# Kernel tuning notes

Hardware: AMD Instinct MI355X
Metric: run time of the kernel (lower is better)

## Reference

```python
import jax, jax.numpy as jnp
import numpy as np

B, LK, D = 32, 2048, 32          # batch, key seq len, input feature dim
LQ = 128                          # number of reference query time points
ET, H = 128, 8                    # embed_time, num_heads
ETK = ET // H
NH = 128                          # nhidden


def setup_inputs() -> dict:
    key = jax.random.key(0)
    ks = jax.random.split(key, 24)
    g = lambda k, shape: jax.random.normal(k, shape, dtype=jnp.float32) * 0.05
    inp = {
        "x": jax.random.normal(ks[0], (B, LK, D), dtype=jnp.float32),
        "time_steps": jax.random.uniform(ks[1], (B, LK), dtype=jnp.float32),
        "query_times": jnp.linspace(0.0, 1.0, LQ, dtype=jnp.float32),
        # learned time embedding: linear(1->1) and periodic(1->ET-1)
        "Wlin": g(ks[2], (1, 1)), "blin": g(ks[3], (1,)),
        "Wper": g(ks[4], (ET - 1, 1)), "bper": g(ks[5], (ET - 1,)),
        # attention projections
        "Wq": g(ks[6], (ET, ET)), "bq": g(ks[7], (ET,)),
        "Wk": g(ks[8], (ET, ET)), "bk": g(ks[9], (ET,)),
        "Wo": g(ks[10], (NH, D * H)), "bo": g(ks[11], (NH,)),
        # GRU (single layer, input NH -> hidden NH), gate order r,z,n
        "W_ih": g(ks[12], (3 * NH, NH)), "b_ih": g(ks[13], (3 * NH,)),
        "W_hh": g(ks[14], (3 * NH, NH)), "b_hh": g(ks[15], (3 * NH,)),
        # classifier MLP NH->300->300->2
        "W1": g(ks[16], (300, NH)), "b1": g(ks[17], (300,)),
        "W2": g(ks[18], (300, 300)), "b2": g(ks[19], (300,)),
        "W3": g(ks[20], (2, 300)), "b3": g(ks[21], (2,)),
    }
    return inp


def _time_embed(tt, Wlin, blin, Wper, bper):
    # tt: (..., L) -> (..., L, ET)
    t = tt[..., None]
    out1 = t @ Wlin.T + blin                  # (..., L, 1)
    out2 = jnp.sin(t @ Wper.T + bper)         # (..., L, ET-1)
    return jnp.concatenate([out1, out2], axis=-1)


def reference(x, time_steps, query_times, Wlin, blin, Wper, bper,
              Wq, bq, Wk, bk, Wo, bo,
              W_ih, b_ih, W_hh, b_hh,
              W1, b1, W2, b2, W3, b3):
    # time embeddings
    k_emb = _time_embed(time_steps, Wlin, blin, Wper, bper)       # (B, LK, ET)
    q_emb = _time_embed(query_times[None, :], Wlin, blin, Wper, bper)  # (1, LQ, ET)

    # multi-head projections
    q = (q_emb @ Wq.T + bq).reshape(1, LQ, H, ETK).transpose(0, 2, 1, 3)   # (1,H,LQ,ETK)
    k = (k_emb @ Wk.T + bk).reshape(B, LK, H, ETK).transpose(0, 2, 1, 3)   # (B,H,LK,ETK)

    # scores broadcast over batch; softmax over keys. Repeating scores over the
    # value feature dim then summing (original code) is mathematically identical
    # to softmax(scores) @ value.
    scores = jnp.einsum("ahqe,bhke->bhqk", q, k) / jnp.sqrt(jnp.float32(ETK))
    p = jax.nn.softmax(scores, axis=-1)                                     # (B,H,LQ,LK)
    att = jnp.einsum("bhqk,bkd->bhqd", p, x)                                # (B,H,LQ,D)
    att = att.transpose(0, 2, 1, 3).reshape(B, LQ, H * D)
    out = att @ Wo.T + bo                                                   # (B,LQ,NH)

    # GRU over LQ steps (PyTorch gate order: r, z, n)
    x_gates = out @ W_ih.T + b_ih                                           # (B,LQ,3NH)
    xs = x_gates.transpose(1, 0, 2)                                         # (LQ,B,3NH)

    def step(h, xg):
        hg = h @ W_hh.T + b_hh
        xr, xz, xn = jnp.split(xg, 3, axis=-1)
        hr, hz, hn = jnp.split(hg, 3, axis=-1)
        r = jax.nn.sigmoid(xr + hr)
        z = jax.nn.sigmoid(xz + hz)
        n = jnp.tanh(xn + r * hn)
        h_new = (1.0 - z) * n + z * h
        return h_new, None

    h0 = jnp.zeros((B, NH), dtype=x.dtype)
    h_last, _ = jax.lax.scan(step, h0, xs)

    # classifier head
    h = jax.nn.relu(h_last @ W1.T + b1)
    h = jax.nn.relu(h @ W2.T + b2)
    return h @ W3.T + b3                                                    # (B,2)
```

## Files before the change

### kernel.cpp

```cpp
#include <hip/hip_runtime.h>
#include <hip/hip_bf16.h>
#include <math.h>

constexpr int Bn  = 32;
constexpr int LK  = 2048;
constexpr int Dn  = 32;
constexpr int LQ  = 128;
constexpr int ET  = 128;
constexpr int Hn  = 8;
constexpr int ETK = 16;
constexpr int NH  = 128;

typedef __attribute__((ext_vector_type(8)))  short bf16x8;
typedef __attribute__((ext_vector_type(16))) float f32x16;

__device__ __forceinline__ float hsum4(float4 v){ return (v.x+v.y)+(v.z+v.w); }
__device__ __forceinline__ void fma4(float4& s, const float4 a, const float4 b){
  s.x = fmaf(a.x,b.x,s.x); s.y = fmaf(a.y,b.y,s.y);
  s.z = fmaf(a.z,b.z,s.z); s.w = fmaf(a.w,b.w,s.w);
}
__device__ __forceinline__ unsigned short bfu(float a){
  __hip_bfloat16 h = __float2bfloat16(a);
  unsigned short u; __builtin_memcpy(&u, &h, 2); return u;
}
__device__ __forceinline__ unsigned pkbf(float a, float b){
  return (unsigned)bfu(a) | ((unsigned)bfu(b) << 16);
}

__global__ __launch_bounds__(256) void xt_kernel(
    const float* __restrict__ x, __hip_bfloat16* __restrict__ xT)
{
  __shared__ float tile[32][65];
  const int wg = blockIdx.x;
  const int b = wg >> 5, kt = wg & 31;
  const int k0 = kt*64;
  const int t = threadIdx.x;
  const float4* src = (const float4*)(x + ((size_t)b*LK + k0)*Dn);
  const float4 v0 = src[t*2], v1 = src[t*2+1];
  const int r = t>>2, c0 = (t&3)*8;
  tile[c0+0][r]=v0.x; tile[c0+1][r]=v0.y; tile[c0+2][r]=v0.z; tile[c0+3][r]=v0.w;
  tile[c0+4][r]=v1.x; tile[c0+5][r]=v1.y; tile[c0+6][r]=v1.z; tile[c0+7][r]=v1.w;
  __syncthreads();
  const int d = t>>3, o = (t&7)*8;
  uint4 w;
  w.x = pkbf(tile[d][o+0], tile[d][o+1]);
  w.y = pkbf(tile[d][o+2], tile[d][o+3]);
  w.z = pkbf(tile[d][o+4], tile[d][o+5]);
  w.w = pkbf(tile[d][o+6], tile[d][o+7]);
  *(uint4*)(xT + ((size_t)(b*Dn + d))*LK + k0 + o) = w;
}

__global__ __launch_bounds__(128) void proj_kernel(
    const float* __restrict__ ts, const float* __restrict__ qt,
    const float* __restrict__ Wlin, const float* __restrict__ blin,
    const float* __restrict__ Wper, const float* __restrict__ bper,
    const float* __restrict__ Wq, const float* __restrict__ bq,
    const float* __restrict__ Wk, const float* __restrict__ bk,
    __hip_bfloat16* __restrict__ Kbuf, __hip_bfloat16* __restrict__ Qbuf)
{
  __shared__ __align__(16) float emb[64*ET];
  const int wg  = blockIdx.x;
  const int tid = threadIdx.x;
  const bool isq = (wg >= 1024);
  const int row0 = isq ? (wg - 1024)*64 : wg*64;
  const float* W    = isq ? Wq : Wk;
  const float* bias = isq ? bq : bk;
  const int op = tid >> 1, half = tid & 1;

  float4 w0[16], w1[16];
  {
    const float4* r0 = (const float4*)(W + (2*op  )*ET + half*64);
    const float4* r1 = (const float4*)(W + (2*op+1)*ET + half*64);
    #pragma unroll
    for (int i=0;i<16;i++){ w0[i]=r0[i]; w1[i]=r1[i]; }
  }
  const float bo = bias[tid];

  const float wl = Wlin[0], bl = blin[0];
  float wp = 0.f, bp = 0.f;
  if (tid > 0){ wp = Wper[tid-1]; bp = bper[tid-1]; }
  for (int r=0;r<64;r++){
    const float t = isq ? qt[row0+r] : ts[row0+r];
    emb[r*ET + tid] = (tid==0) ? fmaf(t, wl, bl) : __sinf(fmaf(t, wp, bp));
  }
  __syncthreads();

  for (int r=0;r<64;r++){
    const float4* e4 = (const float4*)(emb + r*ET + half*64);
    float4 a0 = {0,0,0,0}, a1 = {0,0,0,0};
    #pragma unroll
    for (int i=0;i<16;i++){ const float4 e = e4[i]; fma4(a0, w0[i], e); fma4(a1, w1[i], e); }
    float s0 = hsum4(a0), s1 = hsum4(a1);
    s0 += __shfl_xor(s0, 1);
    s1 += __shfl_xor(s1, 1);
    const float s = (half==0 ? s0 : s1) + bo;
    const int o = tid;
    const int row = row0 + r;
    if (isq){
      Qbuf[((o>>4)*LQ + row)*ETK + (o&15)] = __float2bfloat16(s * 0.25f);
    } else {
      const int b = row >> 11, lkey = row & (LK-1);
      Kbuf[(((b<<3) + (o>>4))*LK + lkey)*ETK + (o&15)] = __float2bfloat16(s);
    }
  }
}

__global__ __launch_bounds__(256, 2) void attn_mfma_kernel(
    const __hip_bfloat16* __restrict__ Kb, const __hip_bfloat16* __restrict__ Qb,
    const __hip_bfloat16* __restrict__ xT, float* __restrict__ attb)
{
  __shared__ uint4 Ks[2][512];
  __shared__ uint4 Xs[2][1024];
  const int wgid = blockIdx.x;
  const int b = wgid >> 3, h = wgid & 7;
  const int tid = threadIdx.x;
  const int lane = tid & 63;
  const int ln = lane & 31, hi = lane >> 5;
  const int q0 = (tid >> 6) * 32;

  bf16x8 qf;
  {
    const uint4 u = *(const uint4*)(Qb + ((h*LQ + q0 + ln)*ETK + 8*hi));
    qf = *(const bf16x8*)&u;
  }

  const f32x16 zf = {0.f,0.f,0.f,0.f,0.f,0.f,0.f,0.f,0.f,0.f,0.f,0.f,0.f,0.f,0.f,0.f};
  f32x16 acc = zf;
  float m = -INFINITY, lsum = 0.f;

  const int sd = tid>>3, skb = (tid&7)*4, sdx = sd&7, ksw = (tid>>2)&7;
  const uint4* Kg = (const uint4*)(Kb + ((size_t)(b*Hn + h)*LK)*ETK);
  const uint4* Xg = (const uint4*)(xT + ((size_t)(b*Dn + sd))*LK + (tid&7)*32);

  uint4 kr0, kr1, xr0, xr1, xr2, xr3;
  {
    const uint4* kp = Kg + tid*2;
    kr0 = kp[0]; kr1 = kp[1];
    xr0 = Xg[0]; xr1 = Xg[1]; xr2 = Xg[2]; xr3 = Xg[3];
    Ks[0][(2*tid  ) ^ ksw] = kr0;
    Ks[0][(2*tid+1) ^ ksw] = kr1;
    Xs[0][sd*32 + ((skb+0)^sdx)] = xr0;
    Xs[0][sd*32 + ((skb+1)^sdx)] = xr1;
    Xs[0][sd*32 + ((skb+2)^sdx)] = xr2;
    Xs[0][sd*32 + ((skb+3)^sdx)] = xr3;
  }
  __syncthreads();

  for (int ck = 0; ck < 8; ck++){
    const int cur = ck & 1, nxt = cur ^ 1;
    if (ck < 7){
      const uint4* kp = Kg + ((ck+1)*256 + tid)*2;
      kr0 = kp[0]; kr1 = kp[1];
      const uint4* xp = Xg + (ck+1)*32;
      xr0 = xp[0]; xr1 = xp[1]; xr2 = xp[2]; xr3 = xp[3];
    }

    for (int kt = 0; kt < 8; kt++){
      const int r = kt*32 + ln;
      const uint4 ku = Ks[cur][(2*r + hi) ^ ((r>>2)&7)];
      const bf16x8 kf = *(const bf16x8*)&ku;
      f32x16 s = __builtin_amdgcn_mfma_f32_32x32x16_bf16(kf, qf, zf, 0, 0, 0);

      float tmax = s[0];
      #pragma unroll
      for (int i=1;i<16;i++) tmax = fmaxf(tmax, s[i]);
      tmax = fmaxf(tmax, __shfl_xor(tmax, 32));
      if (__any(tmax > m)){
        const float mn = fmaxf(m, tmax);
        const float al = __expf(m - mn);
        lsum *= al;
        acc *= al;
        m = mn;
      }
      float p[16]; float tsum = 0.f;
      #pragma unroll
      for (int i=0;i<16;i++){ p[i] = __expf(s[i] - m); tsum += p[i]; }
      tsum += __shfl_xor(tsum, 32);
      lsum += tsum;

      unsigned w0=pkbf(p[0],p[1]),  w1=pkbf(p[2],p[3]),  w2=pkbf(p[4],p[5]),  w3=pkbf(p[6],p[7]);
      unsigned w4=pkbf(p[8],p[9]),  w5=pkbf(p[10],p[11]),w6=pkbf(p[12],p[13]),w7=pkbf(p[14],p[15]);
      unsigned pw0=__shfl_xor(w0,32), pw1=__shfl_xor(w1,32), pw2=__shfl_xor(w2,32), pw3=__shfl_xor(w3,32);
      unsigned pw4=__shfl_xor(w4,32), pw5=__shfl_xor(w5,32), pw6=__shfl_xor(w6,32), pw7=__shfl_xor(w7,32);
      uint4 fa, fb;
      fa.x = hi ? pw2 : w0;  fa.y = hi ? pw3 : w1;
      fa.z = hi ? w2  : pw0; fa.w = hi ? w3  : pw1;
      fb.x = hi ? pw6 : w4;  fb.y = hi ? pw7 : w5;
      fb.z = hi ? w6  : pw4; fb.w = hi ? w7  : pw5;

      const int du = ln*32, dx = ln&7;
      const uint4 xa = Xs[cur][du + ((kt*4 + hi    )^dx)];
      const uint4 xb = Xs[cur][du + ((kt*4 + 2 + hi)^dx)];
      acc = __builtin_amdgcn_mfma_f32_32x32x16_bf16(*(const bf16x8*)&xa, *(const bf16x8*)&fa, acc, 0, 0, 0);
      acc = __builtin_amdgcn_mfma_f32_32x32x16_bf16(*(const bf16x8*)&xb, *(const bf16x8*)&fb, acc, 0, 0, 0);
    }

    if (ck < 7){
      Ks[nxt][(2*tid  ) ^ ksw] = kr0;
      Ks[nxt][(2*tid+1) ^ ksw] = kr1;
      Xs[nxt][sd*32 + ((skb+0)^sdx)] = xr0;
      Xs[nxt][sd*32 + ((skb+1)^sdx)] = xr1;
      Xs[nxt][sd*32 + ((skb+2)^sdx)] = xr2;
      Xs[nxt][sd*32 + ((skb+3)^sdx)] = xr3;
    }
    __syncthreads();
  }

  const float inv = 1.f / lsum;
  float* dst = attb + ((size_t)(b*LQ + q0 + ln)*(Hn*Dn) + h*Dn + 4*hi);
  #pragma unroll
  for (int g=0; g<4; g++){
    float4 v;
    v.x = acc[4*g+0]*inv; v.y = acc[4*g+1]*inv;
    v.z = acc[4*g+2]*inv; v.w = acc[4*g+3]*inv;
    *(float4*)(dst + g*8) = v;
  }
}

__global__ __launch_bounds__(256) void outproj_kernel(
    const float* __restrict__ att, const float* __restrict__ Wo, const float* __restrict__ bo,
    float* __restrict__ outb)
{
  __shared__ __align__(16) float a[16*256];
  const int tid = threadIdx.x;
  const int o = tid>>1, half = tid&1;
  float4 w[32];
  {
    const float4* Wr = (const float4*)(Wo + o*256 + half*128);
    #pragma unroll
    for (int i=0;i<32;i++) w[i]=Wr[i];
  }
  const int row0 = blockIdx.x*16;
  {
    const float4* src = (const float4*)(att + (size_t)row0*256);
    float4* a4 = (float4*)a;
    #pragma unroll
    for (int i=0;i<4;i++) a4[tid + i*256] = src[tid + i*256];
  }
  __syncthreads();
  for (int r=0;r<16;r++){
    const float4* ar = (const float4*)(a + r*256 + half*128);
    float4 s4 = {0,0,0,0};
    #pragma unroll
    for (int i=0;i<32;i++) fma4(s4, w[i], ar[i]);
    float s = hsum4(s4);
    s += __shfl_xor(s, 1);
    if (half==0) outb[(size_t)(row0+r)*NH + o] = s + bo[o];
  }
}

__global__ __launch_bounds__(384) void gates_kernel(
    const float* __restrict__ outb, const float* __restrict__ W_ih, const float* __restrict__ b_ih,
    float* __restrict__ gates)
{
  __shared__ __align__(16) float a[16*128];
  const int tid = threadIdx.x;
  float4 w[32];
  {
    const float4* Wr = (const float4*)(W_ih + (size_t)tid*NH);
    #pragma unroll
    for (int i=0;i<32;i++) w[i]=Wr[i];
  }
  const float bi = b_ih[tid];
  const int row0 = blockIdx.x*16;
  {
    const float4* src = (const float4*)(outb + (size_t)row0*NH);
    float4* a4 = (float4*)a;
    for (int i=tid; i<512; i+=384) a4[i] = src[i];
  }
  __syncthreads();
  for (int r=0;r<16;r++){
    const float4* ar = (const float4*)(a + r*NH);
    float4 s0={0,0,0,0}, s1={0,0,0,0};
    #pragma unroll
    for (int i=0;i<16;i++){ fma4(s0, w[2*i], ar[2*i]); fma4(s1, w[2*i+1], ar[2*i+1]); }
    gates[(size_t)(row0+r)*384 + tid] = hsum4(s0) + hsum4(s1) + bi;
  }
}

__global__ __launch_bounds__(768) void gru_cls_kernel(
    const float* __restrict__ gates, const float* __restrict__ W_hh, const float* __restrict__ b_hh,
    const float* __restrict__ W1, const float* __restrict__ b1,
    const float* __restrict__ W2, const float* __restrict__ b2,
    const float* __restrict__ W3, const float* __restrict__ b3,
    float* __restrict__ out)
{
  __shared__ __align__(16) float h[128];
  __shared__ __align__(16) float hg[384];
  __shared__ __align__(16) float c1[304];
  __shared__ __align__(16) float c2[304];
  const int b = blockIdx.x, t = threadIdx.x;
  const int op = t >> 1, half = t & 1;

  float4 w[16];
  {
    const float4* Wr = (const float4*)(W_hh + (size_t)op*NH + half*64);
    #pragma unroll
    for (int i=0;i<16;i++) w[i]=Wr[i];
  }
  const float bh = b_hh[op];

  float gxr=0.f, gxz=0.f, gxn=0.f;
  if (t < 128){
    const size_t gb = (size_t)b*LQ*384 + t;
    gxr = gates[gb]; gxz = gates[gb+128]; gxn = gates[gb+256];
    h[t] = 0.f;
  }
  __syncthreads();

  for (int tt=0; tt<LQ; tt++){
    float nxr=0.f, nxz=0.f, nxn=0.f;
    if (t < 128 && tt+1 < LQ){
      const size_t nb = ((size_t)b*LQ + tt + 1)*384 + t;
      nxr = gates[nb]; nxz = gates[nb+128]; nxn = gates[nb+256];
    }
    const float4* h4 = ((const float4*)h) + half*16;
    float4 s0={0,0,0,0}, s1={0,0,0,0}, s2={0,0,0,0}, s3={0,0,0,0};
    #pragma unroll
    for (int i=0;i<4;i++){
      fma4(s0, w[4*i  ], h4[4*i  ]);
      fma4(s1, w[4*i+1], h4[4*i+1]);
      fma4(s2, w[4*i+2], h4[4*i+2]);
      fma4(s3, w[4*i+3], h4[4*i+3]);
    }
    s0.x+=s1.x; s0.y+=s1.y; s0.z+=s1.z; s0.w+=s1.w;
    s2.x+=s3.x; s2.y+=s3.y; s2.z+=s3.z; s2.w+=s3.w;
    s0.x+=s2.x; s0.y+=s2.y; s0.z+=s2.z; s0.w+=s2.w;
    float s = hsum4(s0);
    s += __shfl_xor(s, 1);
    if (half==0) hg[op] = s + bh;
    __syncthreads();
    if (t < 128){
      const float r = 1.f/(1.f + __expf(-(gxr + hg[t])));
      const float z = 1.f/(1.f + __expf(-(gxz + hg[t+128])));
      const float n = 1.f - 2.f/(1.f + __expf(2.f*fmaf(r, hg[t+256], gxn)));
      h[t] = (1.f - z)*n + z*h[t];
      gxr = nxr; gxz = nxz; gxn = nxn;
    }
    __syncthreads();
  }

  if (t < 300){
    const float4* Wr1 = (const float4*)(W1 + (size_t)t*128);
    const float4* h4 = (const float4*)h;
    float4 s={0,0,0,0};
    #pragma unroll
    for (int i=0;i<32;i++) fma4(s, Wr1[i], h4[i]);
    c1[t] = fmaxf(hsum4(s) + b1[t], 0.f);
  }
  __syncthreads();
  if (t < 300){
    const float4* Wr2 = (const float4*)(W2 + (size_t)t*300);
    const float4* c14 = (const float4*)c1;
    float4 s={0,0,0,0};
    #pragma unroll
    for (int i=0;i<75;i++) fma4(s, Wr2[i], c14[i]);
    c2[t] = fmaxf(hsum4(s) + b2[t], 0.f);
  }
  __syncthreads();
  if (t < 2){
    const float4* Wr3 = (const float4*)(W3 + (size_t)t*300);
    const float4* c24 = (const float4*)c2;
    float4 s={0,0,0,0};
    #pragma unroll
    for (int i=0;i<75;i++) fma4(s, Wr3[i], c24[i]);
    out[b*2 + t] = hsum4(s) + b3[t];
  }
}

extern "C" void kernel_launch(void* const* d_in, const int* in_sizes, int n_in,
                              void* d_out, int out_size, void* d_ws, size_t ws_size,
                              hipStream_t stream)
{
  const float* x    = (const float*)d_in[0];
  const float* ts   = (const float*)d_in[1];
  const float* qt   = (const float*)d_in[2];
  const float* Wlin = (const float*)d_in[3];
  const float* blin = (const float*)d_in[4];
  const float* Wper = (const float*)d_in[5];
  const float* bper = (const float*)d_in[6];
  const float* Wq   = (const float*)d_in[7];
  const float* bq   = (const float*)d_in[8];
  const float* Wk   = (const float*)d_in[9];
  const float* bk   = (const float*)d_in[10];
  const float* Wo   = (const float*)d_in[11];
  const float* bo   = (const float*)d_in[12];
  const float* W_ih = (const float*)d_in[13];
  const float* b_ih = (const float*)d_in[14];
  const float* W_hh = (const float*)d_in[15];
  const float* b_hh = (const float*)d_in[16];
  const float* W1   = (const float*)d_in[17];
  const float* b1   = (const float*)d_in[18];
  const float* W2   = (const float*)d_in[19];
  const float* b2   = (const float*)d_in[20];
  const float* W3   = (const float*)d_in[21];
  const float* b3   = (const float*)d_in[22];
  float* out = (float*)d_out;

  __hip_bfloat16* Kbb = (__hip_bfloat16*)d_ws;
  __hip_bfloat16* Qbb = Kbb + 8388608;
  __hip_bfloat16* xTb = Qbb + 16384;
  float* attb = (float*)(xTb + 2097152);
  float* outb = attb + 1048576;
  float* gts  = outb + 524288;
  (void)ws_size; (void)in_sizes; (void)n_in; (void)out_size;

  xt_kernel      <<<dim3(1024), dim3(256), 0, stream>>>(x, xTb);
  proj_kernel    <<<dim3(1026), dim3(128), 0, stream>>>(ts, qt, Wlin, blin, Wper, bper, Wq, bq, Wk, bk, Kbb, Qbb);
  attn_mfma_kernel<<<dim3(256), dim3(256), 0, stream>>>(Kbb, Qbb, xTb, attb);
  outproj_kernel <<<dim3(256),  dim3(256), 0, stream>>>(attb, Wo, bo, outb);
  gates_kernel   <<<dim3(256),  dim3(384), 0, stream>>>(outb, W_ih, b_ih, gts);
  gru_cls_kernel <<<dim3(32),   dim3(768), 0, stream>>>(gts, W_hh, b_hh, W1, b1, W2, b2, W3, b3, out);
}
```

Measured before the change: 425.6 us.

## Restructure proj kernel to cache weights in LDS and halve GRU block size

The projection kernel now keeps the full 128x128 Q/K weight matrix in shared memory and holds each thread's embedding rows in registers. Each block processes 128 rows instead of 64, and the grid is halved. The GRU kernel uses 384 threads, one full W_hh row per thread, which removes the cross-lane shuffle reduction from the 128-step serial recurrence. The risks are higher register pressure (32 float4 weights per thread) and fewer blocks for the projection.

```diff
diff --git a/kernel.cpp b/kernel.cpp
--- a/kernel.cpp
+++ b/kernel.cpp
@@ -50,7 +50,7 @@
   *(uint4*)(xT + ((size_t)(b*Dn + d))*LK + k0 + o) = w;
 }
 
-__global__ __launch_bounds__(128) void proj_kernel(
+__global__ __launch_bounds__(128, 2) void proj_kernel(
     const float* __restrict__ ts, const float* __restrict__ qt,
     const float* __restrict__ Wlin, const float* __restrict__ blin,
     const float* __restrict__ Wper, const float* __restrict__ bper,
@@ -58,49 +58,71 @@
     const float* __restrict__ Wk, const float* __restrict__ bk,
     __hip_bfloat16* __restrict__ Kbuf, __hip_bfloat16* __restrict__ Qbuf)
 {
-  __shared__ __align__(16) float emb[64*ET];
+  __shared__ __align__(16) float Wl[ET*ET];
   const int wg  = blockIdx.x;
   const int tid = threadIdx.x;
-  const bool isq = (wg >= 1024);
-  const int row0 = isq ? (wg - 1024)*64 : wg*64;
+  const bool isq = (wg == 512);
+  const int row0 = isq ? 0 : wg*128;
   const float* W    = isq ? Wq : Wk;
   const float* bias = isq ? bq : bk;
-  const int op = tid >> 1, half = tid & 1;
-
-  float4 w0[16], w1[16];
-  {
-    const float4* r0 = (const float4*)(W + (2*op  )*ET + half*64);
-    const float4* r1 = (const float4*)(W + (2*op+1)*ET + half*64);
-    #pragma unroll
-    for (int i=0;i<16;i++){ w0[i]=r0[i]; w1[i]=r1[i]; }
-  }
-  const float bo = bias[tid];
-
-  const float wl = Wlin[0], bl = blin[0];
-  float wp = 0.f, bp = 0.f;
-  if (tid > 0){ wp = Wper[tid-1]; bp = bper[tid-1]; }
-  for (int r=0;r<64;r++){
-    const float t = isq ? qt[row0+r] : ts[row0+r];
-    emb[r*ET + tid] = (tid==0) ? fmaf(t, wl, bl) : __sinf(fmaf(t, wp, bp));
-  }
-  __syncthreads();
-
-  for (int r=0;r<64;r++){
-    const float4* e4 = (const float4*)(emb + r*ET + half*64);
-    float4 a0 = {0,0,0,0}, a1 = {0,0,0,0};
-    #pragma unroll
-    for (int i=0;i<16;i++){ const float4 e = e4[i]; fma4(a0, w0[i], e); fma4(a1, w1[i], e); }
-    float s0 = hsum4(a0), s1 = hsum4(a1);
+  const int r = tid >> 1, half = tid & 1;
+
+  {
+    const float4* Wg4 = (const float4*)W;
+    float4* Wl4 = (float4*)Wl;
+    #pragma unroll
+    for (int i=0;i<32;i++) Wl4[tid + i*128] = Wg4[tid + i*128];
+  }
+
+  const float t0 = isq ? qt[row0+r]      : ts[row0+r];
+  const float t1 = isq ? qt[row0+r+64]   : ts[row0+r+64];
+  float4 e0[16], e1[16];
+  {
+    const float wl0 = Wlin[0], bl0 = blin[0];
+    #pragma unroll
+    for (int i=0;i<16;i++){
+      float a[4], c4[4];
+      #pragma unroll
+      for (int k2=0;k2<4;k2++){
+        const int c = half*64 + i*4 + k2;
+        if (c == 0){ a[k2] = fmaf(t0, wl0, bl0); c4[k2] = fmaf(t1, wl0, bl0); }
+        else {
+          const float wp = Wper[c-1], bp = bper[c-1];
+          a[k2]  = __sinf(fmaf(t0, wp, bp));
+          c4[k2] = __sinf(fmaf(t1, wp, bp));
+        }
+      }
+      e0[i] = make_float4(a[0],a[1],a[2],a[3]);
+      e1[i] = make_float4(c4[0],c4[1],c4[2],c4[3]);
+    }
+  }
+  __syncthreads();
+
+  for (int o=0;o<128;o++){
+    const float4* wr = (const float4*)(Wl + o*ET + half*64);
+    float4 a0={0,0,0,0}, a1={0,0,0,0}, b0={0,0,0,0}, b1={0,0,0,0};
+    #pragma unroll
+    for (int i=0;i<8;i++){
+      const float4 w0 = wr[2*i], w1 = wr[2*i+1];
+      fma4(a0, w0, e0[2*i]); fma4(a1, w1, e0[2*i+1]);
+      fma4(b0, w0, e1[2*i]); fma4(b1, w1, e1[2*i+1]);
+    }
+    float s0 = hsum4(a0) + hsum4(a1);
+    float s1 = hsum4(b0) + hsum4(b1);
     s0 += __shfl_xor(s0, 1);
     s1 += __shfl_xor(s1, 1);
-    const float s = (half==0 ? s0 : s1) + bo;
-    const int o = tid;
-    const int row = row0 + r;
-    if (isq){
-      Qbuf[((o>>4)*LQ + row)*ETK + (o&15)] = __float2bfloat16(s * 0.25f);
-    } else {
-      const int b = row >> 11, lkey = row & (LK-1);
-      Kbuf[(((b<<3) + (o>>4))*LK + lkey)*ETK + (o&15)] = __float2bfloat16(s);
+    if (half == 0){
+      const float bb = bias[o];
+      if (isq){
+        Qbuf[((o>>4)*LQ + r     )*ETK + (o&15)] = __float2bfloat16((s0+bb)*0.25f);
+        Qbuf[((o>>4)*LQ + r + 64)*ETK + (o&15)] = __float2bfloat16((s1+bb)*0.25f);
+      } else {
+        const int row_a = row0 + r, row_b = row0 + r + 64;
+        const int ba = row_a >> 11, la = row_a & (LK-1);
+        const int bb2 = row_b >> 11, lb = row_b & (LK-1);
+        Kbuf[(((ba <<3)+(o>>4))*LK + la)*ETK + (o&15)] = __float2bfloat16(s0+bb);
+        Kbuf[(((bb2<<3)+(o>>4))*LK + lb)*ETK + (o&15)] = __float2bfloat16(s1+bb);
+      }
     }
   }
 }
@@ -217,7 +239,7 @@
   }
 }
 
-__global__ __launch_bounds__(256) void outproj_kernel(
+__global__ __launch_bounds__(256, 1) void outproj_kernel(
     const float* __restrict__ att, const float* __restrict__ Wo, const float* __restrict__ bo,
     float* __restrict__ outb)
 {
@@ -249,7 +271,7 @@
   }
 }
 
-__global__ __launch_bounds__(384) void gates_kernel(
+__global__ __launch_bounds__(384, 1) void gates_kernel(
     const float* __restrict__ outb, const float* __restrict__ W_ih, const float* __restrict__ b_ih,
     float* __restrict__ gates)
 {
@@ -278,7 +300,7 @@
   }
 }
 
-__global__ __launch_bounds__(768) void gru_cls_kernel(
+__global__ __launch_bounds__(384, 1) void gru_cls_kernel(
     const float* __restrict__ gates, const float* __restrict__ W_hh, const float* __restrict__ b_hh,
     const float* __restrict__ W1, const float* __restrict__ b1,
     const float* __restrict__ W2, const float* __restrict__ b2,
@@ -289,82 +311,76 @@
   __shared__ __align__(16) float hg[384];
   __shared__ __align__(16) float c1[304];
   __shared__ __align__(16) float c2[304];
-  const int b = blockIdx.x, t = threadIdx.x;
-  const int op = t >> 1, half = t & 1;
-
-  float4 w[16];
-  {
-    const float4* Wr = (const float4*)(W_hh + (size_t)op*NH + half*64);
-    #pragma unroll
-    for (int i=0;i<16;i++) w[i]=Wr[i];
-  }
-  const float bh = b_hh[op];
+  const int b = blockIdx.x, j = threadIdx.x;
+
+  float4 w[32];
+  {
+    const float4* Wr = (const float4*)(W_hh + (size_t)j*NH);
+    #pragma unroll
+    for (int i=0;i<32;i++) w[i]=Wr[i];
+  }
+  const float bh = b_hh[j];
 
   float gxr=0.f, gxz=0.f, gxn=0.f;
-  if (t < 128){
-    const size_t gb = (size_t)b*LQ*384 + t;
+  if (j < 128){
+    const size_t gb = (size_t)b*LQ*384 + j;
     gxr = gates[gb]; gxz = gates[gb+128]; gxn = gates[gb+256];
-    h[t] = 0.f;
+    h[j] = 0.f;
   }
   __syncthreads();
 
   for (int tt=0; tt<LQ; tt++){
     float nxr=0.f, nxz=0.f, nxn=0.f;
-    if (t < 128 && tt+1 < LQ){
-      const size_t nb = ((size_t)b*LQ + tt + 1)*384 + t;
+    if (j < 128 && tt+1 < LQ){
+      const size_t nb = ((size_t)b*LQ + tt + 1)*384 + j;
       nxr = gates[nb]; nxz = gates[nb+128]; nxn = gates[nb+256];
     }
-    const float4* h4 = ((const float4*)h) + half*16;
+    const float4* h4 = (const float4*)h;
     float4 s0={0,0,0,0}, s1={0,0,0,0}, s2={0,0,0,0}, s3={0,0,0,0};
     #pragma unroll
-    for (int i=0;i<4;i++){
+    for (int i=0;i<8;i++){
       fma4(s0, w[4*i  ], h4[4*i  ]);
       fma4(s1, w[4*i+1], h4[4*i+1]);
       fma4(s2, w[4*i+2], h4[4*i+2]);
       fma4(s3, w[4*i+3], h4[4*i+3]);
     }
-    s0.x+=s1.x; s0.y+=s1.y; s0.z+=s1.z; s0.w+=s1.w;
-    s2.x+=s3.x; s2.y+=s3.y; s2.z+=s3.z; s2.w+=s3.w;
-    s0.x+=s2.x; s0.y+=s2.y; s0.z+=s2.z; s0.w+=s2.w;
-    float s = hsum4(s0);
-    s += __shfl_xor(s, 1);
-    if (half==0) hg[op] = s + bh;
+    hg[j] = (hsum4(s0)+hsum4(s1)) + (hsum4(s2)+hsum4(s3)) + bh;
     __syncthreads();
-    if (t < 128){
-      const float r = 1.f/(1.f + __expf(-(gxr + hg[t])));
-      const float z = 1.f/(1.f + __expf(-(gxz + hg[t+128])));
-      const float n = 1.f - 2.f/(1.f + __expf(2.f*fmaf(r, hg[t+256], gxn)));
-      h[t] = (1.f - z)*n + z*h[t];
+    if (j < 128){
+      const float r = 1.f/(1.f + __expf(-(gxr + hg[j])));
+      const float z = 1.f/(1.f + __expf(-(gxz + hg[j+128])));
+      const float n = 1.f - 2.f/(1.f + __expf(2.f*fmaf(r, hg[j+256], gxn)));
+      h[j] = (1.f - z)*n + z*h[j];
       gxr = nxr; gxz = nxz; gxn = nxn;
     }
     __syncthreads();
   }
 
-  if (t < 300){
-    const float4* Wr1 = (const float4*)(W1 + (size_t)t*128);
+  if (j < 300){
+    const float4* Wr1 = (const float4*)(W1 + (size_t)j*128);
     const float4* h4 = (const float4*)h;
     float4 s={0,0,0,0};
     #pragma unroll
     for (int i=0;i<32;i++) fma4(s, Wr1[i], h4[i]);
-    c1[t] = fmaxf(hsum4(s) + b1[t], 0.f);
-  }
-  __syncthreads();
-  if (t < 300){
-    const float4* Wr2 = (const float4*)(W2 + (size_t)t*300);
+    c1[j] = fmaxf(hsum4(s) + b1[j], 0.f);
+  }
+  __syncthreads();
+  if (j < 300){
+    const float4* Wr2 = (const float4*)(W2 + (size_t)j*300);
     const float4* c14 = (const float4*)c1;
     float4 s={0,0,0,0};
     #pragma unroll
     for (int i=0;i<75;i++) fma4(s, Wr2[i], c14[i]);
-    c2[t] = fmaxf(hsum4(s) + b2[t], 0.f);
-  }
-  __syncthreads();
-  if (t < 2){
-    const float4* Wr3 = (const float4*)(W3 + (size_t)t*300);
+    c2[j] = fmaxf(hsum4(s) + b2[j], 0.f);
+  }
+  __syncthreads();
+  if (j < 2){
+    const float4* Wr3 = (const float4*)(W3 + (size_t)j*300);
     const float4* c24 = (const float4*)c2;
     float4 s={0,0,0,0};
     #pragma unroll
     for (int i=0;i<75;i++) fma4(s, Wr3[i], c24[i]);
-    out[b*2 + t] = hsum4(s) + b3[t];
+    out[b*2 + j] = hsum4(s) + b3[j];
   }
 }
 
@@ -406,9 +422,9 @@
   (void)ws_size; (void)in_sizes; (void)n_in; (void)out_size;
 
   xt_kernel      <<<dim3(1024), dim3(256), 0, stream>>>(x, xTb);
-  proj_kernel    <<<dim3(1026), dim3(128), 0, stream>>>(ts, qt, Wlin, blin, Wper, bper, Wq, bq, Wk, bk, Kbb, Qbb);
+  proj_kernel    <<<dim3(513),  dim3(128), 0, stream>>>(ts, qt, Wlin, blin, Wper, bper, Wq, bq, Wk, bk, Kbb, Qbb);
   attn_mfma_kernel<<<dim3(256), dim3(256), 0, stream>>>(Kbb, Qbb, xTb, attb);
   outproj_kernel <<<dim3(256),  dim3(256), 0, stream>>>(attb, Wo, bo, outb);
   gates_kernel   <<<dim3(256),  dim3(384), 0, stream>>>(outb, W_ih, b_ih, gts);
-  gru_cls_kernel <<<dim3(32),   dim3(768), 0, stream>>>(gts, W_hh, b_hh, W1, b1, W2, b2, W3, b3, out);
-}
+  gru_cls_kernel <<<dim3(32),   dim3(384), 0, stream>>>(gts, W_hh, b_hh, W1, b1, W2, b2, W3, b3, out);
+}
```

Measured after the change: 497.2 us. 1.17x slower.

## Restructure GRU recurrence to one thread per hidden unit with readlane broadcast

Applied to the files above, without the earlier changes.

The GRU kernel now uses 128 threads per batch, one per hidden unit. Each thread holds its three W_hh rows in registers (384 floats) and broadcasts h from LDS via readlane, so the second barrier and the hg shared buffer are gone. Steps ping-pong between two h buffers and need one __syncthreads per step, with gate inputs prefetched two steps ahead. This shortens the serial per-step chain, but the very high register use risks spills, and the per-thread FMA count rises from 64 to 384.

```diff
diff --git a/kernel.cpp b/kernel.cpp
--- a/kernel.cpp
+++ b/kernel.cpp
@@ -25,6 +25,9 @@
 }
 __device__ __forceinline__ unsigned pkbf(float a, float b){
   return (unsigned)bfu(a) | ((unsigned)bfu(b) << 16);
+}
+__device__ __forceinline__ float rdlane(float v, int l){
+  return __uint_as_float(__builtin_amdgcn_readlane(__float_as_uint(v), l));
 }
 
 __global__ __launch_bounds__(256) void xt_kernel(
@@ -278,93 +281,99 @@
   }
 }
 
-__global__ __launch_bounds__(768) void gru_cls_kernel(
+__global__ __launch_bounds__(128, 1) void gru_cls_kernel(
     const float* __restrict__ gates, const float* __restrict__ W_hh, const float* __restrict__ b_hh,
     const float* __restrict__ W1, const float* __restrict__ b1,
     const float* __restrict__ W2, const float* __restrict__ b2,
     const float* __restrict__ W3, const float* __restrict__ b3,
     float* __restrict__ out)
 {
-  __shared__ __align__(16) float h[128];
-  __shared__ __align__(16) float hg[384];
+  __shared__ __align__(16) float h0s[128];
+  __shared__ __align__(16) float h1s[128];
   __shared__ __align__(16) float c1[304];
   __shared__ __align__(16) float c2[304];
-  const int b = blockIdx.x, t = threadIdx.x;
-  const int op = t >> 1, half = t & 1;
-
-  float4 w[16];
-  {
-    const float4* Wr = (const float4*)(W_hh + (size_t)op*NH + half*64);
-    #pragma unroll
-    for (int i=0;i<16;i++) w[i]=Wr[i];
-  }
-  const float bh = b_hh[op];
-
-  float gxr=0.f, gxz=0.f, gxn=0.f;
-  if (t < 128){
-    const size_t gb = (size_t)b*LQ*384 + t;
-    gxr = gates[gb]; gxz = gates[gb+128]; gxn = gates[gb+256];
-    h[t] = 0.f;
-  }
-  __syncthreads();
-
-  for (int tt=0; tt<LQ; tt++){
-    float nxr=0.f, nxz=0.f, nxn=0.f;
-    if (t < 128 && tt+1 < LQ){
-      const size_t nb = ((size_t)b*LQ + tt + 1)*384 + t;
-      nxr = gates[nb]; nxz = gates[nb+128]; nxn = gates[nb+256];
-    }
-    const float4* h4 = ((const float4*)h) + half*16;
-    float4 s0={0,0,0,0}, s1={0,0,0,0}, s2={0,0,0,0}, s3={0,0,0,0};
-    #pragma unroll
-    for (int i=0;i<4;i++){
-      fma4(s0, w[4*i  ], h4[4*i  ]);
-      fma4(s1, w[4*i+1], h4[4*i+1]);
-      fma4(s2, w[4*i+2], h4[4*i+2]);
-      fma4(s3, w[4*i+3], h4[4*i+3]);
-    }
-    s0.x+=s1.x; s0.y+=s1.y; s0.z+=s1.z; s0.w+=s1.w;
-    s2.x+=s3.x; s2.y+=s3.y; s2.z+=s3.z; s2.w+=s3.w;
-    s0.x+=s2.x; s0.y+=s2.y; s0.z+=s2.z; s0.w+=s2.w;
-    float s = hsum4(s0);
-    s += __shfl_xor(s, 1);
-    if (half==0) hg[op] = s + bh;
-    __syncthreads();
-    if (t < 128){
-      const float r = 1.f/(1.f + __expf(-(gxr + hg[t])));
-      const float z = 1.f/(1.f + __expf(-(gxz + hg[t+128])));
-      const float n = 1.f - 2.f/(1.f + __expf(2.f*fmaf(r, hg[t+256], gxn)));
-      h[t] = (1.f - z)*n + z*h[t];
-      gxr = nxr; gxz = nxz; gxn = nxn;
-    }
-    __syncthreads();
-  }
-
-  if (t < 300){
-    const float4* Wr1 = (const float4*)(W1 + (size_t)t*128);
-    const float4* h4 = (const float4*)h;
+  const int b = blockIdx.x, j = threadIdx.x;
+  const int lane = j & 63;
+
+  float4 wr_[32], wz_[32], wn_[32];
+  {
+    const float4* Rr = (const float4*)(W_hh + (size_t)j*NH);
+    const float4* Rz = (const float4*)(W_hh + (size_t)(j+128)*NH);
+    const float4* Rn = (const float4*)(W_hh + (size_t)(j+256)*NH);
+    #pragma unroll
+    for (int i=0;i<32;i++){ wr_[i]=Rr[i]; wz_[i]=Rz[i]; wn_[i]=Rn[i]; }
+  }
+  const float bhr = b_hh[j], bhz = b_hh[j+128], bhn = b_hh[j+256];
+
+  const float* gb = gates + (size_t)b*LQ*384 + j;
+  float xrA = gb[0],   xzA = gb[128],     xnA = gb[256];
+  float xrB = gb[384], xzB = gb[384+128], xnB = gb[384+256];
+
+  float hj = 0.f;
+  h0s[j] = 0.f;
+  __syncthreads();
+
+#define GRU_STEP(HIN, XR, XZ, XN, HOUT)                                              \
+  {                                                                                  \
+    const float4 hv = ((const float4*)(HIN))[lane & 31];                             \
+    float ar0=0,ar1=0,ar2=0,ar3=0, az0=0,az1=0,az2=0,az3=0, an0=0,an1=0,an2=0,an3=0; \
+    _Pragma("unroll")                                                                \
+    for (int k=0;k<32;k++){                                                          \
+      const float e0=rdlane(hv.x,k), e1=rdlane(hv.y,k), e2=rdlane(hv.z,k), e3=rdlane(hv.w,k); \
+      ar0=fmaf(e0,wr_[k].x,ar0); ar1=fmaf(e1,wr_[k].y,ar1);                          \
+      ar2=fmaf(e2,wr_[k].z,ar2); ar3=fmaf(e3,wr_[k].w,ar3);                          \
+      az0=fmaf(e0,wz_[k].x,az0); az1=fmaf(e1,wz_[k].y,az1);                          \
+      az2=fmaf(e2,wz_[k].z,az2); az3=fmaf(e3,wz_[k].w,az3);                          \
+      an0=fmaf(e0,wn_[k].x,an0); an1=fmaf(e1,wn_[k].y,an1);                          \
+      an2=fmaf(e2,wn_[k].z,an2); an3=fmaf(e3,wn_[k].w,an3);                          \
+    }                                                                                \
+    const float hgr = (ar0+ar1)+(ar2+ar3) + bhr;                                     \
+    const float hgz = (az0+az1)+(az2+az3) + bhz;                                     \
+    const float hgn = (an0+an1)+(an2+an3) + bhn;                                     \
+    const float r = 1.f/(1.f + __expf(-((XR) + hgr)));                               \
+    const float z = 1.f/(1.f + __expf(-((XZ) + hgz)));                               \
+    const float n = 1.f - 2.f/(1.f + __expf(2.f*fmaf(r, hgn, (XN))));                \
+    hj = (1.f - z)*n + z*hj;                                                         \
+    (HOUT)[j] = hj;                                                                  \
+    __syncthreads();                                                                 \
+  }
+
+  for (int tt=0; tt<LQ; tt+=2){
+    float prA=0.f,pzA=0.f,pnA=0.f, prB=0.f,pzB=0.f,pnB=0.f;
+    if (tt+2 < LQ){ const float* gp = gb + (size_t)(tt+2)*384; prA=gp[0]; pzA=gp[128]; pnA=gp[256]; }
+    if (tt+3 < LQ){ const float* gp = gb + (size_t)(tt+3)*384; prB=gp[0]; pzB=gp[128]; pnB=gp[256]; }
+    GRU_STEP(h0s, xrA, xzA, xnA, h1s)
+    GRU_STEP(h1s, xrB, xzB, xnB, h0s)
+    xrA=prA; xzA=pzA; xnA=pnA;
+    xrB=prB; xzB=pzB; xnB=pnB;
+  }
+#undef GRU_STEP
+
+  for (int o = j; o < 300; o += 128){
+    const float4* Wr1 = (const float4*)(W1 + (size_t)o*128);
+    const float4* h4 = (const float4*)h0s;
     float4 s={0,0,0,0};
     #pragma unroll
     for (int i=0;i<32;i++) fma4(s, Wr1[i], h4[i]);
-    c1[t] = fmaxf(hsum4(s) + b1[t], 0.f);
-  }
-  __syncthreads();
-  if (t < 300){
-    const float4* Wr2 = (const float4*)(W2 + (size_t)t*300);
+    c1[o] = fmaxf(hsum4(s) + b1[o], 0.f);
+  }
+  __syncthreads();
+  for (int o = j; o < 300; o += 128){
+    const float4* Wr2 = (const float4*)(W2 + (size_t)o*300);
     const float4* c14 = (const float4*)c1;
     float4 s={0,0,0,0};
     #pragma unroll
     for (int i=0;i<75;i++) fma4(s, Wr2[i], c14[i]);
-    c2[t] = fmaxf(hsum4(s) + b2[t], 0.f);
-  }
-  __syncthreads();
-  if (t < 2){
-    const float4* Wr3 = (const float4*)(W3 + (size_t)t*300);
+    c2[o] = fmaxf(hsum4(s) + b2[o], 0.f);
+  }
+  __syncthreads();
+  if (j < 2){
+    const float4* Wr3 = (const float4*)(W3 + (size_t)j*300);
     const float4* c24 = (const float4*)c2;
     float4 s={0,0,0,0};
     #pragma unroll
     for (int i=0;i<75;i++) fma4(s, Wr3[i], c24[i]);
-    out[b*2 + t] = hsum4(s) + b3[t];
+    out[b*2 + j] = hsum4(s) + b3[j];
   }
 }
 
@@ -410,5 +419,5 @@
   attn_mfma_kernel<<<dim3(256), dim3(256), 0, stream>>>(Kbb, Qbb, xTb, attb);
   outproj_kernel <<<dim3(256),  dim3(256), 0, stream>>>(attb, Wo, bo, outb);
   gates_kernel   <<<dim3(256),  dim3(384), 0, stream>>>(outb, W_ih, b_ih, gts);
-  gru_cls_kernel <<<dim3(32),   dim3(768), 0, stream>>>(gts, W_hh, b_hh, W1, b1, W2, b2, W3, b3, out);
-}
+  gru_cls_kernel <<<dim3(32),   dim3(128), 0, stream>>>(gts, W_hh, b_hh, W1, b1, W2, b2, W3, b3, out);
+}
```

Measured after the change: 843.8 us. 98.2% more time.
